# Optimization experiments

Hardware: AMD Instinct MI355X
Metric: run time of the kernel (lower is better)

## Reference

```python
import jax, jax.numpy as jnp
import numpy as np

N_NODES = 10000
N_EDGES = 160000
NEG_SLOPE = 0.2


def _gat_layer(x, src, dst, W, a_src, a_dst, bias, concat):
    # x: [N, F_in]; W: [F_in, H*C]; a_src/a_dst: [H, C]; bias: [H*C] or [C]
    N = x.shape[0]
    H, C = a_src.shape
    h = (x @ W).reshape(N, H, C)                       # [N,H,C]
    al_s = jnp.einsum('nhc,hc->nh', h, a_src)          # [N,H]
    al_d = jnp.einsum('nhc,hc->nh', h, a_dst)          # [N,H]
    e = jax.nn.leaky_relu(al_s[src] + al_d[dst], NEG_SLOPE)  # [E,H]
    # segment softmax over incoming edges of each destination node
    m = jax.ops.segment_max(e, dst, num_segments=N)    # [N,H]
    ex = jnp.exp(e - m[dst])
    denom = jax.ops.segment_sum(ex, dst, num_segments=N)
    alpha = ex / (denom[dst] + 1e-16)                  # [E,H]
    msg = h[src] * alpha[:, :, None]                   # [E,H,C]
    out = jax.ops.segment_sum(msg, dst, num_segments=N)  # [N,H,C]
    out = out.reshape(N, H * C) if concat else out.mean(axis=1)
    return out + bias


def setup_inputs() -> dict:
    key = jax.random.key(0)
    ks = jax.random.split(key, 10)
    in_dim, hid, out_dim, heads = 768, 512, 768, 4
    x = jax.random.normal(ks[0], (N_NODES, in_dim), dtype=jnp.float32)
    edge_index = jax.random.randint(ks[1], (2, N_EDGES), 0, N_NODES, dtype=jnp.int64)
    g = lambda k, shape, fan: jax.random.normal(k, shape, jnp.float32) / np.sqrt(fan)
    return {
        'x': x,
        'edge_index': edge_index,
        'W1': g(ks[2], (in_dim, heads * hid), in_dim),
        'att_src1': g(ks[3], (heads, hid), hid),
        'att_dst1': g(ks[4], (heads, hid), hid),
        'b1': jnp.zeros((heads * hid,), jnp.float32),
        'W2': g(ks[5], (heads * hid, out_dim), heads * hid),
        'att_src2': g(ks[6], (1, out_dim), out_dim),
        'att_dst2': g(ks[7], (1, out_dim), out_dim),
        'b2': jnp.zeros((out_dim,), jnp.float32),
    }


def reference(x, edge_index, W1, att_src1, att_dst1, b1, W2, att_src2, att_dst2, b2):
    N = x.shape[0]
    loops = jnp.arange(N, dtype=edge_index.dtype)
    src = jnp.concatenate([edge_index[0], loops])  # PyG GATConv adds self-loops
    dst = jnp.concatenate([edge_index[1], loops])
    h = jax.nn.elu(_gat_layer(x, src, dst, W1, att_src1, att_dst1, b1, concat=True))
    out = _gat_layer(h, src, dst, W2, att_src2, att_dst2, b2, concat=False)
    return out
```

## Files before the change

### kernel.cpp

```cpp
#include <hip/hip_runtime.h>
#include <hip/hip_bf16.h>
#include <math.h>

#define N_NODES 10000
#define N_EDGES0 160000
#define E_TOT (N_EDGES0 + N_NODES)
#define H1 4
#define C1 512
#define F1 2048
#define IN_DIM 768
#define C2 768
#define NEG_SLOPE 0.2f

typedef _Float16 f16x8 __attribute__((ext_vector_type(8)));
typedef _Float16 f16x4 __attribute__((ext_vector_type(4)));
typedef float f32x4 __attribute__((ext_vector_type(4)));

typedef __attribute__((address_space(1))) const void* gas_ptr;
typedef __attribute__((address_space(3))) void* las_ptr;
static __device__ __forceinline__ void gload16(const void* g, void* l) {
  __builtin_amdgcn_global_load_lds((gas_ptr)g, (las_ptr)l, 16, 0, 0);
}

static __device__ __forceinline__ unsigned enc_f(float v) {
  unsigned u = __float_as_uint(v);
  return (u & 0x80000000u) ? ~u : (u | 0x80000000u);
}
static __device__ __forceinline__ float dec_f(unsigned u) {
  return (u & 0x80000000u) ? __uint_as_float(u ^ 0x80000000u)
                           : __uint_as_float(~u);
}

static __device__ __forceinline__ void edge_sd(const int* __restrict__ ei, int e,
                                               int& s, int& d) {
  if (e < N_EDGES0) { s = ei[e]; d = ei[N_EDGES0 + e]; }
  else { s = e - N_EDGES0; d = s; }
}

__global__ void tsplit_k(const float* __restrict__ W, _Float16* __restrict__ hi,
                         _Float16* __restrict__ lo, int K, int N) {
  __shared__ float tile[32][33];
  const int nb = blockIdx.x * 32, kb = blockIdx.y * 32;
  const int tx = threadIdx.x, ty = threadIdx.y;
  for (int r = ty; r < 32; r += 8)
    tile[r][tx] = W[(size_t)(kb + r) * N + nb + tx];
  __syncthreads();
  for (int r = ty; r < 32; r += 8) {
    float v = tile[tx][r];
    _Float16 h = (_Float16)v;
    hi[(size_t)(nb + r) * K + kb + tx] = h;
    lo[(size_t)(nb + r) * K + kb + tx] = (_Float16)(v - (float)h);
  }
}

__global__ void proj_attn_k(const float* __restrict__ W1,
                            const float* __restrict__ as1,
                            const float* __restrict__ ad1,
                            float* __restrict__ ws, float* __restrict__ wd) {
  int wv = (blockIdx.x * blockDim.x + threadIdx.x) >> 6;
  int lane = threadIdx.x & 63;
  if (wv >= H1 * IN_DIM) return;
  int h = wv / IN_DIM, k = wv - h * IN_DIM;
  const float* wrow = W1 + (size_t)k * F1 + h * C1;
  const float* sa = as1 + h * C1;
  const float* da = ad1 + h * C1;
  float ss = 0.f, sd = 0.f;
  for (int c = lane; c < C1; c += 64) {
    float v = wrow[c];
    ss = fmaf(v, sa[c], ss);
    sd = fmaf(v, da[c], sd);
  }
#pragma unroll
  for (int o = 32; o; o >>= 1) { ss += __shfl_xor(ss, o); sd += __shfl_xor(sd, o); }
  if (lane == 0) { ws[(size_t)h * IN_DIM + k] = ss; wd[(size_t)h * IN_DIM + k] = sd; }
}

__global__ void logits1_k(const float* __restrict__ x,
                          const float* __restrict__ ws, const float* __restrict__ wd,
                          float* __restrict__ als, float* __restrict__ ald) {
  int n = (blockIdx.x * blockDim.x + threadIdx.x) >> 6;
  int lane = threadIdx.x & 63;
  if (n >= N_NODES) return;
  const float* xp = x + (size_t)n * IN_DIM;
  float ss[H1] = {0.f, 0.f, 0.f, 0.f}, sd[H1] = {0.f, 0.f, 0.f, 0.f};
  for (int k = lane; k < IN_DIM; k += 64) {
    float xv = xp[k];
#pragma unroll
    for (int h = 0; h < H1; h++) {
      ss[h] = fmaf(xv, ws[h * IN_DIM + k], ss[h]);
      sd[h] = fmaf(xv, wd[h * IN_DIM + k], sd[h]);
    }
  }
#pragma unroll
  for (int h = 0; h < H1; h++)
#pragma unroll
    for (int o = 32; o; o >>= 1) { ss[h] += __shfl_xor(ss[h], o); sd[h] += __shfl_xor(sd[h], o); }
  if (lane == 0) {
#pragma unroll
    for (int h = 0; h < H1; h++) {
      als[(size_t)n * H1 + h] = ss[h];
      ald[(size_t)n * H1 + h] = sd[h];
    }
  }
}

template <bool SPLITOUT>
__global__ __launch_bounds__(256) void gemm_sf16(
    const _Float16* __restrict__ Ahi, const _Float16* __restrict__ Alo,
    const _Float16* __restrict__ Bhi, const _Float16* __restrict__ Blo,
    int M, int N, int K, int lda, int nch,
    float* __restrict__ C, const float* __restrict__ bias,
    _Float16* __restrict__ ohi, _Float16* __restrict__ olo,
    const float* __restrict__ asrc, const float* __restrict__ adst,
    float* __restrict__ als, float* __restrict__ ald, int Hh, int Cdim) {
  __shared__ _Float16 sAh[128 * 32];
  __shared__ _Float16 sAl[128 * 32];
  __shared__ _Float16 sBh[128 * 32];
  __shared__ _Float16 sBl[128 * 32];

  const int t = threadIdx.x;
  const int w = t >> 6, lane = t & 63;
  const int m0 = blockIdx.y * 128, n0 = blockIdx.x * 128;
  const size_t hofs = (size_t)(n0 / nch) * K;

  const int o0 = w * 1024 + lane * 16;
  const int o1 = o0 + 4096;
  const int ma0 = o0 >> 6, cb0 = o0 & 63;
  const int ma1 = o1 >> 6, cb1 = o1 & 63;
  const int rA0 = min(m0 + ma0, M - 1), rA1 = min(m0 + ma1, M - 1);
  const size_t gA0 = (size_t)rA0 * lda + hofs + (cb0 >> 1);
  const size_t gA1 = (size_t)rA1 * lda + hofs + (cb1 >> 1);
  const size_t gB0 = (size_t)(n0 + ma0) * K + (cb0 >> 1);
  const size_t gB1 = (size_t)(n0 + ma1) * K + (cb1 >> 1);

  char* lA0 = (char*)sAh + w * 1024;
  char* lA1 = lA0 + 4096;
  char* lAl0 = (char*)sAl + w * 1024;
  char* lAl1 = lAl0 + 4096;
  char* lB0 = (char*)sBh + w * 1024;
  char* lB1 = lB0 + 4096;
  char* lBl0 = (char*)sBl + w * 1024;
  char* lBl1 = lBl0 + 4096;

  const int wr = w >> 1, wc = w & 1;
  const int lr = lane & 15, lg = lane >> 4;
  const int aoff = (wr * 64 + lr) * 32 + lg * 8;
  const int boff = (wc * 64 + lr) * 32 + lg * 8;

  f32x4 acc[4][4];
#pragma unroll
  for (int i = 0; i < 4; i++)
#pragma unroll
    for (int j = 0; j < 4; j++) acc[i][j] = (f32x4)(0.f);

  for (int k0 = 0; k0 < K; k0 += 32) {
    __syncthreads();
    gload16(Ahi + gA0 + k0, lA0);
    gload16(Ahi + gA1 + k0, lA1);
    gload16(Alo + gA0 + k0, lAl0);
    gload16(Alo + gA1 + k0, lAl1);
    gload16(Bhi + gB0 + k0, lB0);
    gload16(Bhi + gB1 + k0, lB1);
    gload16(Blo + gB0 + k0, lBl0);
    gload16(Blo + gB1 + k0, lBl1);
    __syncthreads();

    f16x8 ah[4], al[4], bh[4], bl[4];
#pragma unroll
    for (int i = 0; i < 4; i++) {
      ah[i] = *(const f16x8*)&sAh[aoff + i * 16 * 32];
      al[i] = *(const f16x8*)&sAl[aoff + i * 16 * 32];
      bh[i] = *(const f16x8*)&sBh[boff + i * 16 * 32];
      bl[i] = *(const f16x8*)&sBl[boff + i * 16 * 32];
    }
#pragma unroll
    for (int i = 0; i < 4; i++)
#pragma unroll
      for (int j = 0; j < 4; j++) {
        acc[i][j] = __builtin_amdgcn_mfma_f32_16x16x32_f16(ah[i], bh[j], acc[i][j], 0, 0, 0);
        acc[i][j] = __builtin_amdgcn_mfma_f32_16x16x32_f16(ah[i], bl[j], acc[i][j], 0, 0, 0);
        acc[i][j] = __builtin_amdgcn_mfma_f32_16x16x32_f16(al[i], bh[j], acc[i][j], 0, 0, 0);
      }
  }

  if constexpr (SPLITOUT) {
#pragma unroll
    for (int j = 0; j < 4; j++) {
      const int col = n0 + wc * 64 + j * 16 + lr;
      const float bv = bias[col];
#pragma unroll
      for (int i = 0; i < 4; i++) {
        const int rbase = m0 + wr * 64 + i * 16 + lg * 4;
#pragma unroll
        for (int r = 0; r < 4; r++) {
          const int row = rbase + r;
          if (row < M) {
            float o = acc[i][j][r] + bv;
            o = o > 0.f ? o : expm1f(o);
            _Float16 hv = (_Float16)o;
            ohi[(size_t)row * N + col] = hv;
            olo[(size_t)row * N + col] = (_Float16)(o - (float)hv);
          }
        }
      }
    }
  } else {
#pragma unroll
    for (int i = 0; i < 4; i++)
#pragma unroll
      for (int j = 0; j < 4; j++) {
        const int col = n0 + wc * 64 + j * 16 + lr;
        const int rbase = m0 + wr * 64 + i * 16 + lg * 4;
#pragma unroll
        for (int r = 0; r < 4; r++) {
          int row = rbase + r;
          if (row < M) C[(size_t)row * N + col] = acc[i][j][r];
        }
      }

    const int head = n0 / Cdim;
    const int cbase = n0 - head * Cdim + wc * 64 + lr;
    float asv[4], adv[4];
#pragma unroll
    for (int j = 0; j < 4; j++) {
      asv[j] = asrc[(size_t)head * Cdim + cbase + j * 16];
      adv[j] = adst[(size_t)head * Cdim + cbase + j * 16];
    }
#pragma unroll
    for (int i = 0; i < 4; i++) {
      const int rbase = m0 + wr * 64 + i * 16 + lg * 4;
#pragma unroll
      for (int r = 0; r < 4; r++) {
        float ss = 0.f, sd = 0.f;
#pragma unroll
        for (int j = 0; j < 4; j++) {
          float v = acc[i][j][r];
          ss = fmaf(v, asv[j], ss);
          sd = fmaf(v, adv[j], sd);
        }
#pragma unroll
        for (int o = 8; o; o >>= 1) {
          ss += __shfl_xor(ss, o);
          sd += __shfl_xor(sd, o);
        }
        if (lr == 0 && rbase + r < M) {
          atomicAdd(&als[(size_t)(rbase + r) * Hh + head], ss);
          atomicAdd(&ald[(size_t)(rbase + r) * Hh + head], sd);
        }
      }
    }
  }
}

__global__ void edge_max_k(const int* __restrict__ ei,
                           const float* __restrict__ als,
                           const float* __restrict__ ald,
                           float* __restrict__ ev, unsigned* __restrict__ menc,
                           int Hh) {
  int idx = blockIdx.x * blockDim.x + threadIdx.x;
  if (idx >= E_TOT * Hh) return;
  int e = idx / Hh, hh = idx - e * Hh;
  int s, d; edge_sd(ei, e, s, d);
  float x = als[s * Hh + hh] + ald[d * Hh + hh];
  float v = x > 0.f ? x : NEG_SLOPE * x;
  ev[idx] = v;
  atomicMax(&menc[d * Hh + hh], enc_f(v));
}

__global__ void edge_exp_k(const int* __restrict__ ei,
                           const unsigned* __restrict__ menc,
                           const float* __restrict__ ev,
                           const int* __restrict__ csr_pos,
                           float* __restrict__ evs, float* __restrict__ denom,
                           int Hh) {
  int idx = blockIdx.x * blockDim.x + threadIdx.x;
  if (idx >= E_TOT * Hh) return;
  int e = idx / Hh, hh = idx - e * Hh;
  int s, d; edge_sd(ei, e, s, d);
  float m = dec_f(menc[d * Hh + hh]);
  float ex = expf(ev[idx] - m);
  evs[(size_t)csr_pos[e] * Hh + hh] = ex;
  atomicAdd(&denom[d * Hh + hh], ex);
}

__global__ void hist_k(const int* __restrict__ ei, int* __restrict__ count) {
  int e = blockIdx.x * blockDim.x + threadIdx.x;
  if (e >= E_TOT) return;
  int s, d; edge_sd(ei, e, s, d);
  atomicAdd(&count[d], 1);
}

__global__ __launch_bounds__(1024) void scan_k(const int* __restrict__ count,
                                               int* __restrict__ rowstart,
                                               int N, int total) {
  __shared__ int sums[1024];
  __shared__ int carry_s;
  int t = threadIdx.x;
  if (t == 0) carry_s = 0;
  __syncthreads();
  for (int base = 0; base < N; base += 1024) {
    int i = base + t;
    int c = (i < N) ? count[i] : 0;
    sums[t] = c;
    __syncthreads();
    for (int off = 1; off < 1024; off <<= 1) {
      int v = (t >= off) ? sums[t - off] : 0;
      __syncthreads();
      sums[t] += v;
      __syncthreads();
    }
    int carry = carry_s;
    if (i < N) rowstart[i] = carry + sums[t] - c;
    __syncthreads();
    if (t == 1023) carry_s = carry + sums[1023];
    __syncthreads();
  }
  if (t == 0) rowstart[N] = total;
}

__global__ void scatter_k(const int* __restrict__ ei,
                          const int* __restrict__ rowstart,
                          int* __restrict__ cursor,
                          int* __restrict__ csr_src, int* __restrict__ csr_pos) {
  int e = blockIdx.x * blockDim.x + threadIdx.x;
  if (e >= E_TOT) return;
  int s, d; edge_sd(ei, e, s, d);
  int pos = rowstart[d] + atomicAdd(&cursor[d], 1);
  csr_src[pos] = s;
  csr_pos[e] = pos;
}

__global__ __launch_bounds__(192) void aggregate_x_k(
    const float* __restrict__ x, const float* __restrict__ evs,
    const float* __restrict__ denom, const int* __restrict__ rowstart,
    const int* __restrict__ csr_src,
    _Float16* __restrict__ ohi, _Float16* __restrict__ olo) {
  const int n = blockIdx.x;
  const int f0 = threadIdx.x * 4;
  float inv[H1];
#pragma unroll
  for (int h = 0; h < H1; h++) inv[h] = 1.f / (denom[n * H1 + h] + 1e-16f);
  float acc[H1][4];
#pragma unroll
  for (int h = 0; h < H1; h++)
#pragma unroll
    for (int q = 0; q < 4; q++) acc[h][q] = 0.f;

  const int j0 = rowstart[n], j1 = rowstart[n + 1];
  int j = j0;
  for (; j + 4 <= j1; j += 4) {
    int sidx[4];
    float4 wv[4], xv[4];
#pragma unroll
    for (int u = 0; u < 4; u++) sidx[u] = csr_src[j + u];
#pragma unroll
    for (int u = 0; u < 4; u++) wv[u] = *(const float4*)&evs[(size_t)(j + u) * H1];
#pragma unroll
    for (int u = 0; u < 4; u++)
      xv[u] = *(const float4*)(x + (size_t)sidx[u] * IN_DIM + f0);
#pragma unroll
    for (int u = 0; u < 4; u++) {
      const float* pw = (const float*)&wv[u];
#pragma unroll
      for (int h = 0; h < H1; h++) {
        acc[h][0] = fmaf(pw[h], xv[u].x, acc[h][0]);
        acc[h][1] = fmaf(pw[h], xv[u].y, acc[h][1]);
        acc[h][2] = fmaf(pw[h], xv[u].z, acc[h][2]);
        acc[h][3] = fmaf(pw[h], xv[u].w, acc[h][3]);
      }
    }
  }
  for (; j < j1; j++) {
    int s = csr_src[j];
    float4 wv = *(const float4*)&evs[(size_t)j * H1];
    float4 xv = *(const float4*)(x + (size_t)s * IN_DIM + f0);
    const float* pw = (const float*)&wv;
#pragma unroll
    for (int h = 0; h < H1; h++) {
      acc[h][0] = fmaf(pw[h], xv.x, acc[h][0]);
      acc[h][1] = fmaf(pw[h], xv.y, acc[h][1]);
      acc[h][2] = fmaf(pw[h], xv.z, acc[h][2]);
      acc[h][3] = fmaf(pw[h], xv.w, acc[h][3]);
    }
  }

#pragma unroll
  for (int h = 0; h < H1; h++) {
    f16x4 h4, l4;
#pragma unroll
    for (int q = 0; q < 4; q++) {
      float o = acc[h][q] * inv[h];
      _Float16 hv = (_Float16)o;
      h4[q] = hv;
      l4[q] = (_Float16)(o - (float)hv);
    }
    *(f16x4*)&ohi[(size_t)n * (H1 * IN_DIM) + h * IN_DIM + f0] = h4;
    *(f16x4*)&olo[(size_t)n * (H1 * IN_DIM) + h * IN_DIM + f0] = l4;
  }
}

template <int FT>
__global__ __launch_bounds__(256) void aggregate_k(
    const float* __restrict__ hsrc, const float* __restrict__ evs,
    const float* __restrict__ denom, const float* __restrict__ bias,
    const int* __restrict__ rowstart, const int* __restrict__ csr_src,
    float* __restrict__ out, int Hh, int C) {
  const int n = blockIdx.x;
  const int t = threadIdx.x;
  const int F = Hh * C;
  const int f0 = t * FT;
  const int hh = f0 / C;
  const float inv = 1.f / (denom[n * Hh + hh] + 1e-16f);
  float acc[FT];
#pragma unroll
  for (int i = 0; i < FT; i++) acc[i] = 0.f;
  const int j0 = rowstart[n], j1 = rowstart[n + 1];

  constexpr int UN = 8;
  int j = j0;
  for (; j + UN <= j1; j += UN) {
    int   sidx[UN];
    float wv[UN];
#pragma unroll
    for (int u = 0; u < UN; u++) sidx[u] = csr_src[j + u];
#pragma unroll
    for (int u = 0; u < UN; u++) wv[u] = evs[(size_t)(j + u) * Hh + hh];
    float4 va[UN][FT / 4];
#pragma unroll
    for (int u = 0; u < UN; u++) {
      const float* hp = hsrc + (size_t)sidx[u] * F + f0;
#pragma unroll
      for (int q = 0; q < FT / 4; q++) va[u][q] = *(const float4*)(hp + q * 4);
    }
#pragma unroll
    for (int u = 0; u < UN; u++)
#pragma unroll
      for (int q = 0; q < FT / 4; q++) {
        acc[q * 4 + 0] = fmaf(wv[u], va[u][q].x, acc[q * 4 + 0]);
        acc[q * 4 + 1] = fmaf(wv[u], va[u][q].y, acc[q * 4 + 1]);
        acc[q * 4 + 2] = fmaf(wv[u], va[u][q].z, acc[q * 4 + 2]);
        acc[q * 4 + 3] = fmaf(wv[u], va[u][q].w, acc[q * 4 + 3]);
      }
  }
  for (; j < j1; j++) {
    int s = csr_src[j];
    float wgt = evs[(size_t)j * Hh + hh];
    const float* hp = hsrc + (size_t)s * F + f0;
#pragma unroll
    for (int q = 0; q < FT / 4; q++) {
      float4 v = *(const float4*)(hp + q * 4);
      acc[q * 4 + 0] = fmaf(wgt, v.x, acc[q * 4 + 0]);
      acc[q * 4 + 1] = fmaf(wgt, v.y, acc[q * 4 + 1]);
      acc[q * 4 + 2] = fmaf(wgt, v.z, acc[q * 4 + 2]);
      acc[q * 4 + 3] = fmaf(wgt, v.w, acc[q * 4 + 3]);
    }
  }
#pragma unroll
  for (int i = 0; i < FT; i++)
    out[(size_t)n * F + f0 + i] = acc[i] * inv + bias[f0 + i];
}

extern "C" void kernel_launch(void* const* d_in, const int* in_sizes, int n_in,
                              void* d_out, int out_size, void* d_ws, size_t ws_size,
                              hipStream_t stream) {
  const float* x   = (const float*)d_in[0];
  const int*   ei  = (const int*)d_in[1];
  const float* W1  = (const float*)d_in[2];
  const float* as1 = (const float*)d_in[3];
  const float* ad1 = (const float*)d_in[4];
  const float* b1  = (const float*)d_in[5];
  const float* W2  = (const float*)d_in[6];
  const float* as2 = (const float*)d_in[7];
  const float* ad2 = (const float*)d_in[8];
  const float* b2  = (const float*)d_in[9];
  float* out = (float*)d_out;

  char* p = (char*)d_ws;
  auto alloc = [&](size_t bytes) {
    char* r = p;
    p += (bytes + 255) & ~(size_t)255;
    return r;
  };
  _Float16* xahi  = (_Float16*)alloc((size_t)N_NODES * H1 * IN_DIM * 2);
  _Float16* xalo  = (_Float16*)alloc((size_t)N_NODES * H1 * IN_DIM * 2);
  _Float16* W1hi  = (_Float16*)alloc((size_t)IN_DIM * F1 * 2);
  _Float16* W1lo  = (_Float16*)alloc((size_t)IN_DIM * F1 * 2);
  _Float16* W2hi  = (_Float16*)alloc((size_t)F1 * C2 * 2);
  _Float16* W2lo  = (_Float16*)alloc((size_t)F1 * C2 * 2);
  _Float16* h2hi  = (_Float16*)alloc((size_t)N_NODES * F1 * 2);
  _Float16* h2lo  = (_Float16*)alloc((size_t)N_NODES * F1 * 2);
  float*    ws1   = (float*)alloc((size_t)H1 * IN_DIM * 4);
  float*    wd1   = (float*)alloc((size_t)H1 * IN_DIM * 4);
  float*    als   = (float*)alloc((size_t)N_NODES * H1 * 4);
  float*    ald   = (float*)alloc((size_t)N_NODES * H1 * 4);
  unsigned* menc  = (unsigned*)alloc((size_t)N_NODES * H1 * 4);
  float*    denom = (float*)alloc((size_t)N_NODES * H1 * 4);
  float*    ev    = (float*)alloc((size_t)E_TOT * H1 * 4);
  float*    evs   = (float*)alloc((size_t)E_TOT * H1 * 4);
  int*      count    = (int*)alloc((size_t)N_NODES * 4);
  int*      rowstart = (int*)alloc((size_t)(N_NODES + 1) * 4);
  int*      cursor   = (int*)alloc((size_t)N_NODES * 4);
  int*      csr_src  = (int*)alloc((size_t)E_TOT * 4);
  int*      csr_pos  = (int*)alloc((size_t)E_TOT * 4);
  float*    h3 = (float*)xahi;

  const int EB = (E_TOT + 255) / 256;

  hipMemsetAsync(count, 0, (size_t)N_NODES * 4, stream);
  hipMemsetAsync(cursor, 0, (size_t)N_NODES * 4, stream);
  hist_k<<<EB, 256, 0, stream>>>(ei, count);
  scan_k<<<1, 1024, 0, stream>>>(count, rowstart, N_NODES, E_TOT);
  scatter_k<<<EB, 256, 0, stream>>>(ei, rowstart, cursor, csr_src, csr_pos);

  tsplit_k<<<dim3(F1 / 32, IN_DIM / 32), dim3(32, 8), 0, stream>>>(W1, W1hi, W1lo,
                                                                   IN_DIM, F1);
  tsplit_k<<<dim3(C2 / 32, F1 / 32), dim3(32, 8), 0, stream>>>(W2, W2hi, W2lo,
                                                               F1, C2);
  proj_attn_k<<<(H1 * IN_DIM * 64) / 256, 256, 0, stream>>>(W1, as1, ad1, ws1, wd1);

  logits1_k<<<(N_NODES * 64 + 255) / 256, 256, 0, stream>>>(x, ws1, wd1, als, ald);
  hipMemsetAsync(menc, 0, (size_t)N_NODES * H1 * 4, stream);
  hipMemsetAsync(denom, 0, (size_t)N_NODES * H1 * 4, stream);
  edge_max_k<<<(E_TOT * H1 + 255) / 256, 256, 0, stream>>>(ei, als, ald, ev, menc, H1);
  edge_exp_k<<<(E_TOT * H1 + 255) / 256, 256, 0, stream>>>(ei, menc, ev, csr_pos,
                                                           evs, denom, H1);
  aggregate_x_k<<<N_NODES, 192, 0, stream>>>(x, evs, denom, rowstart, csr_src,
                                             xahi, xalo);
  gemm_sf16<true><<<dim3(F1 / 128, (N_NODES + 127) / 128), 256, 0, stream>>>(
      xahi, xalo, W1hi, W1lo, N_NODES, F1, IN_DIM, H1 * IN_DIM, C1,
      nullptr, b1, h2hi, h2lo, nullptr, nullptr, nullptr, nullptr, 0, C1);

  hipMemsetAsync(als, 0, (size_t)N_NODES * 4, stream);
  hipMemsetAsync(ald, 0, (size_t)N_NODES * 4, stream);
  gemm_sf16<false><<<dim3(C2 / 128, (N_NODES + 127) / 128), 256, 0, stream>>>(
      h2hi, h2lo, W2hi, W2lo, N_NODES, C2, F1, F1, 1 << 30,
      h3, nullptr, nullptr, nullptr, as2, ad2, als, ald, 1, C2);
  hipMemsetAsync(menc, 0, (size_t)N_NODES * 4, stream);
  hipMemsetAsync(denom, 0, (size_t)N_NODES * 4, stream);
  edge_max_k<<<EB, 256, 0, stream>>>(ei, als, ald, ev, menc, 1);
  edge_exp_k<<<EB, 256, 0, stream>>>(ei, menc, ev, csr_pos, evs, denom, 1);
  aggregate_k<4><<<N_NODES, 192, 0, stream>>>(h3, evs, denom, b2, rowstart,
                                              csr_src, out, 1, C2);
}
```

Before: 640.6 us.

## Double GEMM K-step, swizzle LDS layout, and remap workgroups across XCDs

The split-fp16 GEMM now loads a 64-wide K slice per iteration instead of 32, which halves the number of barrier pairs per tile. The LDS tile rows use an XOR-style rotation of the 16-byte chunks to avoid bank conflicts on the MFMA fragment reads. The 2D grid becomes a 1D grid whose block index is remapped so consecutive tiles land on the same XCD, aiming for better L2 reuse. LDS usage doubles to 64 KB per block, which may reduce occupancy.

```diff
diff --git a/kernel.cpp b/kernel.cpp
--- a/kernel.cpp
+++ b/kernel.cpp
@@ -108,44 +108,39 @@
 __global__ __launch_bounds__(256) void gemm_sf16(
     const _Float16* __restrict__ Ahi, const _Float16* __restrict__ Alo,
     const _Float16* __restrict__ Bhi, const _Float16* __restrict__ Blo,
-    int M, int N, int K, int lda, int nch,
+    int M, int N, int K, int lda, int nch, int nbx, int nwg,
     float* __restrict__ C, const float* __restrict__ bias,
     _Float16* __restrict__ ohi, _Float16* __restrict__ olo,
     const float* __restrict__ asrc, const float* __restrict__ adst,
     float* __restrict__ als, float* __restrict__ ald, int Hh, int Cdim) {
-  __shared__ _Float16 sAh[128 * 32];
-  __shared__ _Float16 sAl[128 * 32];
-  __shared__ _Float16 sBh[128 * 32];
-  __shared__ _Float16 sBl[128 * 32];
+  __shared__ _Float16 sAh[128 * 64];
+  __shared__ _Float16 sAl[128 * 64];
+  __shared__ _Float16 sBh[128 * 64];
+  __shared__ _Float16 sBl[128 * 64];
+
+  const int orig = blockIdx.x;
+  const int q = nwg >> 3, rr = nwg & 7;
+  const int xcd = orig & 7, pos = orig >> 3;
+  const int wgid = (xcd < rr ? xcd * (q + 1) : rr * (q + 1) + (xcd - rr) * q) + pos;
+  const int bx = wgid % nbx, by = wgid / nbx;
+  const int m0 = by * 128, n0 = bx * 128;
 
   const int t = threadIdx.x;
   const int w = t >> 6, lane = t & 63;
-  const int m0 = blockIdx.y * 128, n0 = blockIdx.x * 128;
   const size_t hofs = (size_t)(n0 / nch) * K;
 
-  const int o0 = w * 1024 + lane * 16;
-  const int o1 = o0 + 4096;
-  const int ma0 = o0 >> 6, cb0 = o0 & 63;
-  const int ma1 = o1 >> 6, cb1 = o1 & 63;
-  const int rA0 = min(m0 + ma0, M - 1), rA1 = min(m0 + ma1, M - 1);
-  const size_t gA0 = (size_t)rA0 * lda + hofs + (cb0 >> 1);
-  const size_t gA1 = (size_t)rA1 * lda + hofs + (cb1 >> 1);
-  const size_t gB0 = (size_t)(n0 + ma0) * K + (cb0 >> 1);
-  const size_t gB1 = (size_t)(n0 + ma1) * K + (cb1 >> 1);
-
-  char* lA0 = (char*)sAh + w * 1024;
-  char* lA1 = lA0 + 4096;
-  char* lAl0 = (char*)sAl + w * 1024;
-  char* lAl1 = lAl0 + 4096;
-  char* lB0 = (char*)sBh + w * 1024;
-  char* lB1 = lB0 + 4096;
-  char* lBl0 = (char*)sBl + w * 1024;
-  char* lBl1 = lBl0 + 4096;
+  const int gsrc = ((lane & 7) - (lane >> 3)) & 7;
+  const int ru = w * 8 + (lane >> 3);
+  size_t gA[4], gB[4];
+#pragma unroll
+  for (int i = 0; i < 4; i++) {
+    const int ra = min(m0 + i * 32 + ru, M - 1);
+    gA[i] = (size_t)ra * lda + hofs + gsrc * 8;
+    gB[i] = (size_t)(n0 + i * 32 + ru) * K + gsrc * 8;
+  }
 
   const int wr = w >> 1, wc = w & 1;
   const int lr = lane & 15, lg = lane >> 4;
-  const int aoff = (wr * 64 + lr) * 32 + lg * 8;
-  const int boff = (wc * 64 + lr) * 32 + lg * 8;
 
   f32x4 acc[4][4];
 #pragma unroll
@@ -153,34 +148,40 @@
 #pragma unroll
     for (int j = 0; j < 4; j++) acc[i][j] = (f32x4)(0.f);
 
-  for (int k0 = 0; k0 < K; k0 += 32) {
+  for (int k0 = 0; k0 < K; k0 += 64) {
     __syncthreads();
-    gload16(Ahi + gA0 + k0, lA0);
-    gload16(Ahi + gA1 + k0, lA1);
-    gload16(Alo + gA0 + k0, lAl0);
-    gload16(Alo + gA1 + k0, lAl1);
-    gload16(Bhi + gB0 + k0, lB0);
-    gload16(Bhi + gB1 + k0, lB1);
-    gload16(Blo + gB0 + k0, lBl0);
-    gload16(Blo + gB1 + k0, lBl1);
+#pragma unroll
+    for (int i = 0; i < 4; i++) {
+      const int lofs = w * 1024 + i * 4096;
+      gload16(Ahi + gA[i] + k0, (char*)sAh + lofs);
+      gload16(Alo + gA[i] + k0, (char*)sAl + lofs);
+      gload16(Bhi + gB[i] + k0, (char*)sBh + lofs);
+      gload16(Blo + gB[i] + k0, (char*)sBl + lofs);
+    }
     __syncthreads();
 
-    f16x8 ah[4], al[4], bh[4], bl[4];
-#pragma unroll
-    for (int i = 0; i < 4; i++) {
-      ah[i] = *(const f16x8*)&sAh[aoff + i * 16 * 32];
-      al[i] = *(const f16x8*)&sAl[aoff + i * 16 * 32];
-      bh[i] = *(const f16x8*)&sBh[boff + i * 16 * 32];
-      bl[i] = *(const f16x8*)&sBl[boff + i * 16 * 32];
-    }
-#pragma unroll
-    for (int i = 0; i < 4; i++)
-#pragma unroll
-      for (int j = 0; j < 4; j++) {
-        acc[i][j] = __builtin_amdgcn_mfma_f32_16x16x32_f16(ah[i], bh[j], acc[i][j], 0, 0, 0);
-        acc[i][j] = __builtin_amdgcn_mfma_f32_16x16x32_f16(ah[i], bl[j], acc[i][j], 0, 0, 0);
-        acc[i][j] = __builtin_amdgcn_mfma_f32_16x16x32_f16(al[i], bh[j], acc[i][j], 0, 0, 0);
+#pragma unroll
+    for (int kk = 0; kk < 2; kk++) {
+      const int ga = ((kk * 4 + lg + (lr & 7)) & 7) * 8;
+      f16x8 ah[4], al[4], bh[4], bl[4];
+#pragma unroll
+      for (int i = 0; i < 4; i++) {
+        const int ao = (wr * 64 + i * 16 + lr) * 64 + ga;
+        const int bo = (wc * 64 + i * 16 + lr) * 64 + ga;
+        ah[i] = *(const f16x8*)&sAh[ao];
+        al[i] = *(const f16x8*)&sAl[ao];
+        bh[i] = *(const f16x8*)&sBh[bo];
+        bl[i] = *(const f16x8*)&sBl[bo];
       }
+#pragma unroll
+      for (int i = 0; i < 4; i++)
+#pragma unroll
+        for (int j = 0; j < 4; j++) {
+          acc[i][j] = __builtin_amdgcn_mfma_f32_16x16x32_f16(ah[i], bh[j], acc[i][j], 0, 0, 0);
+          acc[i][j] = __builtin_amdgcn_mfma_f32_16x16x32_f16(ah[i], bl[j], acc[i][j], 0, 0, 0);
+          acc[i][j] = __builtin_amdgcn_mfma_f32_16x16x32_f16(al[i], bh[j], acc[i][j], 0, 0, 0);
+        }
+    }
   }
 
   if constexpr (SPLITOUT) {
@@ -505,6 +506,7 @@
   float*    h3 = (float*)xahi;
 
   const int EB = (E_TOT + 255) / 256;
+  const int MT = (N_NODES + 127) / 128;
 
   hipMemsetAsync(count, 0, (size_t)N_NODES * 4, stream);
   hipMemsetAsync(cursor, 0, (size_t)N_NODES * 4, stream);
@@ -526,15 +528,21 @@
                                                            evs, denom, H1);
   aggregate_x_k<<<N_NODES, 192, 0, stream>>>(x, evs, denom, rowstart, csr_src,
                                              xahi, xalo);
-  gemm_sf16<true><<<dim3(F1 / 128, (N_NODES + 127) / 128), 256, 0, stream>>>(
-      xahi, xalo, W1hi, W1lo, N_NODES, F1, IN_DIM, H1 * IN_DIM, C1,
-      nullptr, b1, h2hi, h2lo, nullptr, nullptr, nullptr, nullptr, 0, C1);
+  {
+    const int nbx = F1 / 128, nwg = nbx * MT;
+    gemm_sf16<true><<<nwg, 256, 0, stream>>>(
+        xahi, xalo, W1hi, W1lo, N_NODES, F1, IN_DIM, H1 * IN_DIM, C1, nbx, nwg,
+        nullptr, b1, h2hi, h2lo, nullptr, nullptr, nullptr, nullptr, 0, C1);
+  }
 
   hipMemsetAsync(als, 0, (size_t)N_NODES * 4, stream);
   hipMemsetAsync(ald, 0, (size_t)N_NODES * 4, stream);
-  gemm_sf16<false><<<dim3(C2 / 128, (N_NODES + 127) / 128), 256, 0, stream>>>(
-      h2hi, h2lo, W2hi, W2lo, N_NODES, C2, F1, F1, 1 << 30,
-      h3, nullptr, nullptr, nullptr, as2, ad2, als, ald, 1, C2);
+  {
+    const int nbx = C2 / 128, nwg = nbx * MT;
+    gemm_sf16<false><<<nwg, 256, 0, stream>>>(
+        h2hi, h2lo, W2hi, W2lo, N_NODES, C2, F1, F1, 1 << 30, nbx, nwg,
+        h3, nullptr, nullptr, nullptr, as2, ad2, als, ald, 1, C2);
+  }
   hipMemsetAsync(menc, 0, (size_t)N_NODES * 4, stream);
   hipMemsetAsync(denom, 0, (size_t)N_NODES * 4, stream);
   edge_max_k<<<EB, 256, 0, stream>>>(ei, als, ald, ev, menc, 1);
```

After: 614.6 us. 4.1% less time.
